# Kernel optimization log

Measured on AMD Instinct MI355X. Metric: run time of the kernel, lower is better.

## Reference

```python
import jax, jax.numpy as jnp
import numpy as np

D_IN = 512
D_OUT = 512
NUM_HEADS = 8
HEAD_DIM = D_OUT // NUM_HEADS


def setup_inputs() -> dict:
    key = jax.random.key(0)
    ks = jax.random.split(key, 6)
    b, t, n = 4, 32, 256
    scale = 1.0 / np.sqrt(D_IN)
    return {
        "x": jax.random.normal(ks[0], (b, t, n, D_IN), dtype=jnp.float32),
        "Wq": jax.random.normal(ks[1], (D_IN, D_OUT), dtype=jnp.float32) * scale,
        "Wk": jax.random.normal(ks[2], (D_IN, D_OUT), dtype=jnp.float32) * scale,
        "Wv": jax.random.normal(ks[3], (D_IN, D_OUT), dtype=jnp.float32) * scale,
        "Wo": jax.random.normal(ks[4], (D_OUT, D_OUT), dtype=jnp.float32) * scale,
        "bo": jax.random.normal(ks[5], (D_OUT,), dtype=jnp.float32) * 0.01,
    }


def reference(x, Wq, Wk, Wv, Wo, bo):
    b, t, n, _ = x.shape
    h, hd = NUM_HEADS, HEAD_DIM
    # QKV projections (no bias, qkv_bias=False)
    q = (x @ Wq).reshape(b, t, n, h, hd)
    k = (x @ Wk).reshape(b, t, n, h, hd)
    v = (x @ Wv).reshape(b, t, n, h, hd)
    # attention over tokens, per (batch, timestamp, head)
    scores = jnp.einsum('btqhd,btkhd->bthqk', q, k) / np.sqrt(hd).astype(jnp.float32)
    weights = jax.nn.softmax(scores, axis=-1)
    # dropout p=0.0 (eval / deterministic reference) -> identity
    ctx = jnp.einsum('bthqk,btkhd->btqhd', weights, v).reshape(b, t, n, D_OUT)
    return ctx @ Wo + bo
```

## Files before the change

kernel.cpp:

```cpp
#include <hip/hip_runtime.h>
#include <hip/hip_bf16.h>

typedef __attribute__((ext_vector_type(8))) short bf16x8;
typedef __attribute__((ext_vector_type(4))) float f32x4;

#define MFMA_16x16x32(a,b,c) __builtin_amdgcn_mfma_f32_16x16x32_bf16((a),(b),(c),0,0,0)

__device__ __forceinline__ unsigned short f2bf(float f){
  unsigned int u = __float_as_uint(f);
  u += 0x7FFFu + ((u >> 16) & 1u);
  return (unsigned short)(u >> 16);
}

__device__ __forceinline__ unsigned int cvtpk_bf16(float lo, float hi){
  unsigned int r;
  asm("v_cvt_pk_bf16_f32 %0, %1, %2" : "=v"(r) : "v"(lo), "v"(hi));
  return r;
}

__device__ __forceinline__ void async16(const void* g, void* l){
  __builtin_amdgcn_global_load_lds((const __attribute__((address_space(1))) void*)g,
                                   (__attribute__((address_space(3))) void*)l,
                                   16, 0, 0);
}

#define FENCE asm volatile("" ::: "memory")
#define BARR  do{ FENCE; __builtin_amdgcn_s_barrier(); FENCE; }while(0)
#define BARRL do{ asm volatile("s_waitcnt lgkmcnt(0)" ::: "memory"); \
                  __builtin_amdgcn_s_barrier(); FENCE; }while(0)

__global__ __launch_bounds__(256) void convert_all(const float* __restrict__ x,
                                                   const float* __restrict__ Wq,
                                                   const float* __restrict__ Wk,
                                                   const float* __restrict__ Wv,
                                                   const float* __restrict__ Wo,
                                                   unsigned short* __restrict__ xb,
                                                   unsigned short* __restrict__ WqkvT,
                                                   unsigned short* __restrict__ WoT){
  int idx = blockIdx.x*256 + threadIdx.x;
  int stride = gridDim.x*256;
  const int n4 = 16777216/4;
  for (int i = idx; i < n4; i += stride){
    float4 v = reinterpret_cast<const float4*>(x)[i];
    ushort4 o;
    o.x = f2bf(v.x); o.y = f2bf(v.y); o.z = f2bf(v.z); o.w = f2bf(v.w);
    reinterpret_cast<ushort4*>(xb)[i] = o;
  }
  const int T1 = 1536*512;
  const int total = T1 + 512*512;
  for (int o = idx; o < total; o += stride){
    if (o < T1){
      int n = o >> 9, k = o & 511;
      const float* W = (n < 512) ? Wq : ((n < 1024) ? Wk : Wv);
      WqkvT[o] = f2bf(W[k*512 + (n & 511)]);
    } else {
      int o2 = o - T1;
      int n = o2 >> 9, k = o2 & 511;
      WoT[o2] = f2bf(Wo[k*512 + n]);
    }
  }
}

template<bool BIAS, bool OUTBF16>
__global__ __launch_bounds__(512, 2) void gemm4(const unsigned short* __restrict__ A,
                                                const unsigned short* __restrict__ Bt,
                                                float* __restrict__ Cf, unsigned short* __restrict__ Cb,
                                                const float* __restrict__ bias,
                                                int K, int NB, int ldc){
  __shared__ __attribute__((aligned(16))) char ldsA[2][16384];
  __shared__ __attribute__((aligned(16))) char ldsB[2][16384];
  const int tid = threadIdx.x;
  const int lane = tid & 63, w = tid >> 6;
  const int wr = w >> 1, wc = w & 1;
  const int l15 = lane & 15, lhi = lane >> 4;

  const int cpx = gridDim.x >> 3;
  const int bid = (blockIdx.x & 7) * cpx + (blockIdx.x >> 3);
  const int bm = bid / NB, bn = bid % NB;

  const int row0 = tid >> 3;
  const int srcb = ((tid & 7) << 4) ^ ((row0 & 7) << 4);
  const size_t rK2 = (size_t)K * 2;
  const char* Ab = (const char*)(A + (size_t)(bm*128 + row0) * K) + srcb;
  const char* Bb = (const char*)(Bt + (size_t)(bn*128 + row0) * K) + srcb;

#define STG_A(p,kt) do{ _Pragma("unroll") for (int j=0;j<2;++j) \
    async16(Ab + (size_t)(j*64)*rK2 + (size_t)(kt)*2, ldsA[p] + j*8192 + w*1024); }while(0)
#define STG_B(p,kt) do{ _Pragma("unroll") for (int j=0;j<2;++j) \
    async16(Bb + (size_t)(j*64)*rK2 + (size_t)(kt)*2, ldsB[p] + j*8192 + w*1024); }while(0)

#define LDAF(p) do{ _Pragma("unroll") for (int f=0;f<2;++f){ \
    const int m_ = wr*32 + f*16 + l15; \
    const char* base_ = ldsA[p] + m_*128; \
    af[f][0] = *reinterpret_cast<const bf16x8*>(base_ + (((lhi<<4))      ^ ((m_&7)<<4))); \
    af[f][1] = *reinterpret_cast<const bf16x8*>(base_ + ((64 + (lhi<<4)) ^ ((m_&7)<<4))); } }while(0)
#define LDBF(dst, p, nh) do{ _Pragma("unroll") for (int n2=0;n2<2;++n2){ \
    const int n_ = wc*64 + ((nh)*2+n2)*16 + l15; \
    const char* base_ = ldsB[p] + n_*128; \
    dst[n2][0] = *reinterpret_cast<const bf16x8*>(base_ + (((lhi<<4))      ^ ((n_&7)<<4))); \
    dst[n2][1] = *reinterpret_cast<const bf16x8*>(base_ + ((64 + (lhi<<4)) ^ ((n_&7)<<4))); } }while(0)
#define MFQ(nh, B_) do{ _Pragma("unroll") for (int f=0;f<2;++f) \
    _Pragma("unroll") for (int n2=0;n2<2;++n2) \
    _Pragma("unroll") for (int kk=0;kk<2;++kk) \
      acc[f][(nh)*2+n2] = MFMA_16x16x32(af[f][kk], B_[n2][kk], acc[f][(nh)*2+n2]); }while(0)

  f32x4 acc[2][4];
  const f32x4 fzero = {0.f,0.f,0.f,0.f};
  #pragma unroll
  for (int i=0;i<2;++i)
    #pragma unroll
    for (int j=0;j<4;++j) acc[i][j] = fzero;
  bf16x8 af[2][2], bf0[2][2], bfc[2][2];
  const int nt = K >> 6;

  STG_A(0,0); STG_B(0,0); STG_A(1,64); STG_B(1,64);
  asm volatile("s_waitcnt vmcnt(4)" ::: "memory");
  __builtin_amdgcn_s_barrier(); FENCE;

  for (int t = 0; t < nt; ++t){
    const int p = t & 1;
    const int kt2 = (t+2) << 6;
    LDAF(p); LDBF(bf0, p, 0); LDBF(bfc, p, 1);
    __builtin_amdgcn_s_setprio(1); MFQ(0, bf0); __builtin_amdgcn_s_setprio(0);
    BARRL;
    if (t+2 < nt){ STG_A(p, kt2); STG_B(p, kt2); }
    __builtin_amdgcn_s_setprio(1); MFQ(1, bfc); __builtin_amdgcn_s_setprio(0);
    if (t+1 < nt){
      if (t+2 < nt) asm volatile("s_waitcnt vmcnt(4) lgkmcnt(0)" ::: "memory");
      else          asm volatile("s_waitcnt vmcnt(0) lgkmcnt(0)" ::: "memory");
      __builtin_amdgcn_s_barrier(); FENCE;
    }
  }

  #pragma unroll
  for (int mi=0;mi<2;++mi){
    const int r = bm*128 + wr*32 + mi*16 + lhi*4;
    #pragma unroll
    for (int ni=0;ni<4;++ni){
      const int cc = bn*128 + wc*64 + ni*16 + l15;
      float bv = 0.f;
      if (BIAS) bv = bias[cc];
      #pragma unroll
      for (int i=0;i<4;++i){
        float v = acc[mi][ni][i] + bv;
        if (OUTBF16) Cb[(size_t)(r+i)*ldc + cc] = f2bf(v);
        else         Cf[(size_t)(r+i)*ldc + cc] = v;
      }
    }
  }
#undef STG_A
#undef STG_B
#undef LDAF
#undef LDBF
#undef MFQ
}

__global__ __launch_bounds__(256) void attn_kernel(const unsigned short* __restrict__ qkv,
                                                   unsigned short* __restrict__ ctx){
  __shared__ __attribute__((aligned(16))) unsigned short Ks[256*64];
  __shared__ __attribute__((aligned(16))) unsigned short Vst[64*264];

  const int bid = blockIdx.x;
  const int h = bid & 7, bt = bid >> 3;
  const int r0 = bt << 8;
  const int tid = threadIdx.x;
  const int lane = tid & 63, w = tid >> 6;
  const int l15 = lane & 15, lhi = lane >> 4;
  const char* qkvB = (const char*)qkv;
  const f32x4 fzero = {0.f,0.f,0.f,0.f};

  bf16x8 qf[4][2];
  #pragma unroll
  for (int st=0; st<4; ++st){
    int q0 = w*64 + st*16;
    #pragma unroll
    for (int kk=0; kk<2; ++kk)
      qf[st][kk] = *reinterpret_cast<const bf16x8*>(
          qkvB + ((size_t)(r0 + q0 + l15)*1536 + h*64 + kk*32 + lhi*8)*2);
  }

  #pragma unroll
  for (int j=0;j<8;++j){
    int c = (w*8+j)*64 + lane;
    int tok = c >> 3;
    int src = ((c & 7) << 4) ^ ((tok & 7) << 4);
    async16(qkvB + ((size_t)(r0 + tok)*1536 + 512 + h*64)*2 + src,
            (char*)Ks + ((w*8+j) << 10));
  }
  {
    const char* vbase = qkvB + ((size_t)(r0 + tid)*1536 + 1024 + h*64)*2;
    #pragma unroll
    for (int j=0;j<8;++j){
      bf16x8 vv = *reinterpret_cast<const bf16x8*>(vbase + (j<<4));
      #pragma unroll
      for (int e=0;e<8;++e)
        Vst[(j*8+e)*264 + tid] = (unsigned short)vv[e];
    }
  }
  __syncthreads();

  const int ga2 = (lhi & 1) << 1;
  const int lA = l15 + (ga2 << 4);
  const int lB = lA + 16;
  const bool odd = (lhi >> 1) != 0;

  #pragma unroll
  for (int st=0; st<4; ++st){
    const int q0 = w*64 + st*16;

    f32x4 S[16];
    #pragma unroll
    for (int t=0;t<16;++t) S[t] = fzero;
    #pragma unroll
    for (int kk=0;kk<2;++kk){
      #pragma unroll
      for (int t=0;t<16;++t){
        int tok = t*16 + l15;
        int off = tok*128 + (((kk<<6) + (lhi<<4)) ^ ((tok & 7) << 4));
        bf16x8 kf = *reinterpret_cast<const bf16x8*>((const char*)Ks + off);
        S[t] = MFMA_16x16x32(kf, qf[st][kk], S[t]);
      }
    }

    float m = S[0][0];
    #pragma unroll
    for (int t=0;t<16;++t)
      #pragma unroll
      for (int i=0;i<4;++i) m = fmaxf(m, S[t][i]);
    m = fmaxf(m, __shfl_xor(m, 16));
    m = fmaxf(m, __shfl_xor(m, 32));

    float l = 0.f;
    unsigned int P2[32];
    #pragma unroll
    for (int t=0;t<16;++t){
      float p0 = __expf((S[t][0] - m) * 0.125f);
      float p1 = __expf((S[t][1] - m) * 0.125f);
      float p2 = __expf((S[t][2] - m) * 0.125f);
      float p3 = __expf((S[t][3] - m) * 0.125f);
      l += (p0 + p1) + (p2 + p3);
      P2[2*t]   = cvtpk_bf16(p0, p1);
      P2[2*t+1] = cvtpk_bf16(p2, p3);
    }
    l += __shfl_xor(l, 16);
    l += __shfl_xor(l, 32);
    float rl = 1.0f / l;

    f32x4 O[4];
    #pragma unroll
    for (int dt=0;dt<4;++dt) O[dt] = fzero;
    #pragma unroll
    for (int s=0;s<8;++s){
      unsigned int a0e = __shfl((int)P2[4*s+0], lA), a0o = __shfl((int)P2[4*s+2], lA);
      unsigned int a1e = __shfl((int)P2[4*s+1], lA), a1o = __shfl((int)P2[4*s+3], lA);
      unsigned int b0e = __shfl((int)P2[4*s+0], lB), b0o = __shfl((int)P2[4*s+2], lB);
      unsigned int b1e = __shfl((int)P2[4*s+1], lB), b1o = __shfl((int)P2[4*s+3], lB);
      unsigned int u0 = odd ? a0o : a0e;
      unsigned int u1 = odd ? a1o : a1e;
      unsigned int u2 = odd ? b0o : b0e;
      unsigned int u3 = odd ? b1o : b1e;
      bf16x8 pa;
      reinterpret_cast<unsigned int*>(&pa)[0] = u0;
      reinterpret_cast<unsigned int*>(&pa)[1] = u1;
      reinterpret_cast<unsigned int*>(&pa)[2] = u2;
      reinterpret_cast<unsigned int*>(&pa)[3] = u3;
      #pragma unroll
      for (int dt=0;dt<4;++dt){
        bf16x8 vb = *reinterpret_cast<const bf16x8*>(&Vst[(dt*16 + l15)*264 + s*32 + 8*lhi]);
        O[dt] = MFMA_16x16x32(pa, vb, O[dt]);
      }
    }

    float rl4[4];
    #pragma unroll
    for (int i=0;i<4;++i) rl4[i] = __shfl(rl, lhi*4 + i);
    #pragma unroll
    for (int dt=0;dt<4;++dt){
      int col = h*64 + dt*16 + l15;
      #pragma unroll
      for (int i=0;i<4;++i){
        int row = r0 + q0 + lhi*4 + i;
        ctx[(size_t)row*512 + col] = f2bf(O[dt][i] * rl4[i]);
      }
    }
  }
}

extern "C" void kernel_launch(void* const* d_in, const int* in_sizes, int n_in,
                              void* d_out, int out_size, void* d_ws, size_t ws_size,
                              hipStream_t stream) {
  const float* x  = (const float*)d_in[0];
  const float* Wq = (const float*)d_in[1];
  const float* Wk = (const float*)d_in[2];
  const float* Wv = (const float*)d_in[3];
  const float* Wo = (const float*)d_in[4];
  const float* bo = (const float*)d_in[5];
  float* out = (float*)d_out;

  char* ws = (char*)d_ws;
  unsigned short* xb    = (unsigned short*)ws;
  unsigned short* qkv   = (unsigned short*)(ws + 33554432);
  unsigned short* WqkvT = (unsigned short*)(ws + 134217728);
  unsigned short* WoT   = (unsigned short*)(ws + 135790592);
  unsigned short* ctx   = xb;

  convert_all<<<2048, 256, 0, stream>>>(x, Wq, Wk, Wv, Wo, xb, WqkvT, WoT);
  gemm4<false, true><<<3072, 512, 0, stream>>>(xb, WqkvT, nullptr, qkv, nullptr, 512, 12, 1536);
  attn_kernel<<<1024, 256, 0, stream>>>(qkv, ctx);
  gemm4<true, false><<<1024, 512, 0, stream>>>(ctx, WoT, out, nullptr, bo, 512, 4, 512);
}
```

Baseline: 162.3 us.

## Fuse fp32-to-bf16 conversion of x into the QKV GEMM A-tile loads

Drops the separate pass that converted the whole x tensor to bf16 in workspace. The QKV GEMM now loads fp32 x tiles into registers, converts them with packed bf16 conversion and writes them swizzled into LDS, prefetching one tile ahead. This avoids a full write and reread of a 32 MB intermediate. The cost is that each 128-column N tile re-reads fp32 A, which is twice the bytes of bf16, and the A pipeline now goes through registers with a full vmcnt(0) wait every iteration.

```diff
diff --git a/kernel.cpp b/kernel.cpp
--- a/kernel.cpp
+++ b/kernel.cpp
@@ -25,27 +25,17 @@
 }
 
 #define FENCE asm volatile("" ::: "memory")
-#define BARR  do{ FENCE; __builtin_amdgcn_s_barrier(); FENCE; }while(0)
 #define BARRL do{ asm volatile("s_waitcnt lgkmcnt(0)" ::: "memory"); \
                   __builtin_amdgcn_s_barrier(); FENCE; }while(0)
 
-__global__ __launch_bounds__(256) void convert_all(const float* __restrict__ x,
-                                                   const float* __restrict__ Wq,
-                                                   const float* __restrict__ Wk,
-                                                   const float* __restrict__ Wv,
-                                                   const float* __restrict__ Wo,
-                                                   unsigned short* __restrict__ xb,
-                                                   unsigned short* __restrict__ WqkvT,
-                                                   unsigned short* __restrict__ WoT){
+__global__ __launch_bounds__(256) void prep_weights(const float* __restrict__ Wq,
+                                                    const float* __restrict__ Wk,
+                                                    const float* __restrict__ Wv,
+                                                    const float* __restrict__ Wo,
+                                                    unsigned short* __restrict__ WqkvT,
+                                                    unsigned short* __restrict__ WoT){
   int idx = blockIdx.x*256 + threadIdx.x;
   int stride = gridDim.x*256;
-  const int n4 = 16777216/4;
-  for (int i = idx; i < n4; i += stride){
-    float4 v = reinterpret_cast<const float4*>(x)[i];
-    ushort4 o;
-    o.x = f2bf(v.x); o.y = f2bf(v.y); o.z = f2bf(v.z); o.w = f2bf(v.w);
-    reinterpret_cast<ushort4*>(xb)[i] = o;
-  }
   const int T1 = 1536*512;
   const int total = T1 + 512*512;
   for (int o = idx; o < total; o += stride){
@@ -61,8 +51,8 @@
   }
 }
 
-template<bool BIAS, bool OUTBF16>
-__global__ __launch_bounds__(512, 2) void gemm4(const unsigned short* __restrict__ A,
+template<bool AFP32, bool BIAS, bool OUTBF16>
+__global__ __launch_bounds__(512, 2) void gemm4(const void* __restrict__ Av,
                                                 const unsigned short* __restrict__ Bt,
                                                 float* __restrict__ Cf, unsigned short* __restrict__ Cb,
                                                 const float* __restrict__ bias,
@@ -81,13 +71,28 @@
   const int row0 = tid >> 3;
   const int srcb = ((tid & 7) << 4) ^ ((row0 & 7) << 4);
   const size_t rK2 = (size_t)K * 2;
-  const char* Ab = (const char*)(A + (size_t)(bm*128 + row0) * K) + srcb;
-  const char* Bb = (const char*)(Bt + (size_t)(bn*128 + row0) * K) + srcb;
-
-#define STG_A(p,kt) do{ _Pragma("unroll") for (int j=0;j<2;++j) \
+  const unsigned short* A16 = (const unsigned short*)Av;
+  const float*          A32 = (const float*)Av;
+  const char* Ab = (const char*)(A16 + (size_t)(bm*128 + row0) * K) + srcb;
+  const char* Bb = (const char*)(Bt  + (size_t)(bn*128 + row0) * K) + srcb;
+
+  const int arow = (w << 4) + (lhi << 2);
+  const int au = l15;
+  const float* xbase = A32 + (size_t)(bm*128 + arow) * K + au*4;
+
+#define STG_A16(p,kt) do{ _Pragma("unroll") for (int j=0;j<2;++j) \
     async16(Ab + (size_t)(j*64)*rK2 + (size_t)(kt)*2, ldsA[p] + j*8192 + w*1024); }while(0)
 #define STG_B(p,kt) do{ _Pragma("unroll") for (int j=0;j<2;++j) \
     async16(Bb + (size_t)(j*64)*rK2 + (size_t)(kt)*2, ldsB[p] + j*8192 + w*1024); }while(0)
+
+#define LDA_G(dst, kt) do{ _Pragma("unroll") for (int j=0;j<4;++j) \
+    dst[j] = *reinterpret_cast<const float4*>(xbase + (size_t)j*K + (kt)); }while(0)
+#define WRA(p, src) do{ _Pragma("unroll") for (int j=0;j<4;++j){ \
+    const int r_ = arow + j; \
+    char* pw_ = ldsA[p] + r_*128 + ((((au>>1) ^ (r_&7))<<4) + ((au&1)<<3)); \
+    uint2 v_; v_.x = cvtpk_bf16(src[j].x, src[j].y); \
+              v_.y = cvtpk_bf16(src[j].z, src[j].w); \
+    *reinterpret_cast<uint2*>(pw_) = v_; } }while(0)
 
 #define LDAF(p) do{ _Pragma("unroll") for (int f=0;f<2;++f){ \
     const int m_ = wr*32 + f*16 + l15; \
@@ -111,24 +116,46 @@
     #pragma unroll
     for (int j=0;j<4;++j) acc[i][j] = fzero;
   bf16x8 af[2][2], bf0[2][2], bfc[2][2];
+  float4 areg[4];
   const int nt = K >> 6;
 
-  STG_A(0,0); STG_B(0,0); STG_A(1,64); STG_B(1,64);
-  asm volatile("s_waitcnt vmcnt(4)" ::: "memory");
-  __builtin_amdgcn_s_barrier(); FENCE;
+  if constexpr (AFP32){
+    float4 a0[4], a1[4];
+    LDA_G(a0, 0); LDA_G(a1, 64);
+    STG_B(0, 0); STG_B(1, 64);
+    asm volatile("s_waitcnt vmcnt(8)" ::: "memory");
+    WRA(0, a0);
+    asm volatile("s_waitcnt vmcnt(2)" ::: "memory");
+    WRA(1, a1);
+    if (nt > 2) LDA_G(areg, 128);
+    asm volatile("s_waitcnt lgkmcnt(0)" ::: "memory");
+    __builtin_amdgcn_s_barrier(); FENCE;
+  } else {
+    STG_A16(0,0); STG_B(0,0); STG_A16(1,64); STG_B(1,64);
+    asm volatile("s_waitcnt vmcnt(4)" ::: "memory");
+    __builtin_amdgcn_s_barrier(); FENCE;
+  }
 
   for (int t = 0; t < nt; ++t){
     const int p = t & 1;
-    const int kt2 = (t+2) << 6;
+    const int kt2 = (t+2) << 6, kt3 = (t+3) << 6;
     LDAF(p); LDBF(bf0, p, 0); LDBF(bfc, p, 1);
     __builtin_amdgcn_s_setprio(1); MFQ(0, bf0); __builtin_amdgcn_s_setprio(0);
     BARRL;
-    if (t+2 < nt){ STG_A(p, kt2); STG_B(p, kt2); }
-    __builtin_amdgcn_s_setprio(1); MFQ(1, bfc); __builtin_amdgcn_s_setprio(0);
-    if (t+1 < nt){
-      if (t+2 < nt) asm volatile("s_waitcnt vmcnt(4) lgkmcnt(0)" ::: "memory");
-      else          asm volatile("s_waitcnt vmcnt(0) lgkmcnt(0)" ::: "memory");
-      __builtin_amdgcn_s_barrier(); FENCE;
+    if constexpr (AFP32){
+      asm volatile("s_waitcnt vmcnt(0)" ::: "memory");
+      if (t+2 < nt){ WRA(p, areg); STG_B(p, kt2); }
+      if (t+3 < nt) LDA_G(areg, kt3);
+      __builtin_amdgcn_s_setprio(1); MFQ(1, bfc); __builtin_amdgcn_s_setprio(0);
+      if (t+1 < nt) BARRL;
+    } else {
+      if (t+2 < nt){ STG_A16(p, kt2); STG_B(p, kt2); }
+      __builtin_amdgcn_s_setprio(1); MFQ(1, bfc); __builtin_amdgcn_s_setprio(0);
+      if (t+1 < nt){
+        if (t+2 < nt) asm volatile("s_waitcnt vmcnt(4) lgkmcnt(0)" ::: "memory");
+        else          asm volatile("s_waitcnt vmcnt(0) lgkmcnt(0)" ::: "memory");
+        __builtin_amdgcn_s_barrier(); FENCE;
+      }
     }
   }
 
@@ -148,8 +175,10 @@
       }
     }
   }
-#undef STG_A
+#undef STG_A16
 #undef STG_B
+#undef LDA_G
+#undef WRA
 #undef LDAF
 #undef LDBF
 #undef MFQ
@@ -298,14 +327,15 @@
   float* out = (float*)d_out;
 
   char* ws = (char*)d_ws;
-  unsigned short* xb    = (unsigned short*)ws;
+  unsigned short* ctx   = (unsigned short*)ws;
   unsigned short* qkv   = (unsigned short*)(ws + 33554432);
   unsigned short* WqkvT = (unsigned short*)(ws + 134217728);
   unsigned short* WoT   = (unsigned short*)(ws + 135790592);
-  unsigned short* ctx   = xb;
-
-  convert_all<<<2048, 256, 0, stream>>>(x, Wq, Wk, Wv, Wo, xb, WqkvT, WoT);
-  gemm4<false, true><<<3072, 512, 0, stream>>>(xb, WqkvT, nullptr, qkv, nullptr, 512, 12, 1536);
+
+  prep_weights<<<512, 256, 0, stream>>>(Wq, Wk, Wv, Wo, WqkvT, WoT);
+  gemm4<true, false, true><<<3072, 512, 0, stream>>>(x, WqkvT, nullptr, qkv, nullptr,
+                                                     512, 12, 1536);
   attn_kernel<<<1024, 256, 0, stream>>>(qkv, ctx);
-  gemm4<true, false><<<1024, 512, 0, stream>>>(ctx, WoT, out, nullptr, bo, 512, 4, 512);
-}
+  gemm4<false, true, false><<<1024, 512, 0, stream>>>(ctx, WoT, out, nullptr, bo,
+                                                      512, 4, 512);
+}
```

Result: slower. 172.7 us (+6.5%).
